# Kernel optimization log

Measured on AMD Instinct MI355X. Metric: run time of the kernel, lower is better.

The kernel has to match this reference:

```python
import jax, jax.numpy as jnp
import numpy as np

D_MODEL = 1024
NUM_HEADS = 16
BATCH = 2
SEQ = 2048


def _trunc_normal(key, shape, std):
    # truncated normal on [-3std, 3std], matching torch.nn.init.trunc_normal_
    return jax.random.truncated_normal(key, -3.0, 3.0, shape, dtype=jnp.float32) * std


def setup_inputs() -> dict:
    key = jax.random.key(0)
    kx, kq, kk, kv, ko = jax.random.split(key, 5)
    std = (2.0 / (D_MODEL + D_MODEL)) ** 0.5
    return {
        "X": jax.random.normal(kx, (BATCH, SEQ, D_MODEL), dtype=jnp.float32),
        "q_proj": _trunc_normal(kq, (D_MODEL, D_MODEL), std),
        "k_proj": _trunc_normal(kk, (D_MODEL, D_MODEL), std),
        "v_proj": _trunc_normal(kv, (D_MODEL, D_MODEL), std),
        "o_proj": _trunc_normal(ko, (D_MODEL, D_MODEL), std),
    }


def reference(X, q_proj, k_proj, v_proj, o_proj):
    B, S, D = X.shape
    H = NUM_HEADS
    d_k = D // H

    # weights stored as (d_model, d_model); split output dim into heads
    q_w = q_proj.reshape(H, d_k, D)        # heads d_k d_model
    k_w = k_proj.reshape(H, d_k, D)
    v_w = v_proj.reshape(H, d_k, D)
    o_w = o_proj.reshape(D, H, d_k).transpose(1, 0, 2)  # heads d_model d_v

    q = jnp.einsum('hkd,bsd->bhsk', q_w, X)  # [B,H,S,d_k]
    k = jnp.einsum('hkd,bsd->bhsk', k_w, X)
    v = jnp.einsum('hkd,bsd->bhsk', v_w, X)

    scale = 1.0 / jnp.sqrt(jnp.asarray(d_k, dtype=X.dtype))
    scores = jnp.einsum('bhqk,bhsk->bhqs', q, k) * scale  # [B,H,S,S]
    causal = jnp.tril(jnp.ones((S, S), dtype=bool))
    scores = jnp.where(causal, scores, jnp.asarray(-jnp.inf, dtype=scores.dtype))
    attn = jax.nn.softmax(scores, axis=-1)
    attn_out = jnp.einsum('bhqs,bhsk->bhqk', attn, v)  # [B,H,S,d_v]

    return jnp.einsum('hdv,bhsv->bsd', o_w, attn_out)  # [B,S,d_model]
```

## Files before the change

### kernel.cpp

```cpp
#include <hip/hip_runtime.h>

typedef unsigned short u16;
typedef __bf16 bf16x8 __attribute__((ext_vector_type(8)));
typedef float f32x4 __attribute__((ext_vector_type(4)));
typedef u16 u16x8 __attribute__((ext_vector_type(8)));
typedef u16 u16x4v __attribute__((ext_vector_type(4)));

#define D_MODEL 1024
#define SEQ 2048
#define NB 2
#define NH 16

#define MFMA(a, b, c) __builtin_amdgcn_mfma_f32_16x16x32_bf16(a, b, c, 0, 0, 0)

__device__ __forceinline__ u16 f2bf(float f) {
  unsigned u = __builtin_bit_cast(unsigned, f);
  u += 0x7FFFu + ((u >> 16) & 1u);
  return (u16)(u >> 16);
}

__device__ __forceinline__ u16 f2bf_hw(float f) {
  return __builtin_bit_cast(u16, (__bf16)f);
}

__device__ __forceinline__ bf16x8 ld8(const u16* p) {
  return __builtin_bit_cast(bf16x8, *(const u16x8*)p);
}

typedef const __attribute__((address_space(1))) unsigned gu32;
typedef __attribute__((address_space(3))) unsigned lu32;
__device__ __forceinline__ void gload16(const u16* g, u16* l) {
  __builtin_amdgcn_global_load_lds((gu32*)g, (lu32*)l, 16, 0, 0);
}

__global__ __launch_bounds__(256) void convert_kernel(
    const float* __restrict__ X, const float* __restrict__ Wq,
    const float* __restrict__ Wk, const float* __restrict__ Wv,
    const float* __restrict__ Wo, u16* __restrict__ Xb, u16* __restrict__ Wb)
{
  const int NX4 = 1024 * 1024;
  const int NW4 = 256 * 1024;
  const int TOT = NX4 + 4 * NW4;
  for (int i = blockIdx.x * 256 + threadIdx.x; i < TOT; i += gridDim.x * 256) {
    const float* src;
    u16* dst;
    if (i < NX4) {
      src = X + (size_t)i * 4;
      dst = Xb + (size_t)i * 4;
    } else {
      int j = i - NX4;
      int w = j >> 18;
      int off = j & (NW4 - 1);
      const float* ws = (w == 0) ? Wq : (w == 1) ? Wk : (w == 2) ? Wv : Wo;
      src = ws + (size_t)off * 4;
      dst = Wb + (size_t)j * 4;
    }
    float4 v = *(const float4*)src;
    u16x4v o = { f2bf(v.x), f2bf(v.y), f2bf(v.z), f2bf(v.w) };
    *(u16x4v*)dst = o;
  }
}

template<int MODE>
__global__ __launch_bounds__(256) void gemm128(
    const u16* __restrict__ A, const u16* __restrict__ B,
    u16* __restrict__ Qb, u16* __restrict__ Kb, u16* __restrict__ Vt,
    float* __restrict__ out)
{
  __shared__ u16 As[2][128 * 64];
  __shared__ u16 Bs[2][128 * 64];
  const int t = threadIdx.x;
  const int lane = t & 63, w = t >> 6;
  const int wr = w >> 1, wc = w & 1;
  const int m0 = blockIdx.x * 128;
  const int n0 = blockIdx.y * 128;
  const int kg = lane >> 4, lr = lane & 15;
  const int lrow = lane >> 3, lch = lane & 7;

  f32x4 acc[4][4] = {};

  auto stage = [&](int buf, int kt) {
    #pragma unroll
    for (int i = 0; i < 4; ++i) {
      int row = (w * 4 + i) * 8 + lrow;
      int sch = lch ^ (row & 7);
      gload16(&A[(size_t)(m0 + row) * 1024 + kt * 64 + sch * 8], &As[buf][(w * 4 + i) * 512]);
      gload16(&B[(size_t)(n0 + row) * 1024 + kt * 64 + sch * 8], &Bs[buf][(w * 4 + i) * 512]);
    }
  };

  stage(0, 0);
  __syncthreads();
  int cur = 0;

  for (int kt = 0; kt < 16; ++kt) {
    if (kt + 1 < 16) stage(cur ^ 1, kt + 1);

    const u16* as = &As[cur][0];
    const u16* bs = &Bs[cur][0];
    #pragma unroll
    for (int kh = 0; kh < 2; ++kh) {
      bf16x8 a[4], b[4];
      #pragma unroll
      for (int mi = 0; mi < 4; ++mi) {
        int row = wr * 64 + mi * 16 + lr;
        int ch = (kh * 4 + kg) ^ (lr & 7);
        a[mi] = ld8(&as[row * 64 + ch * 8]);
      }
      #pragma unroll
      for (int ni = 0; ni < 4; ++ni) {
        int row = wc * 64 + ni * 16 + lr;
        int ch = (kh * 4 + kg) ^ (lr & 7);
        b[ni] = ld8(&bs[row * 64 + ch * 8]);
      }
      #pragma unroll
      for (int mi = 0; mi < 4; ++mi)
        #pragma unroll
        for (int ni = 0; ni < 4; ++ni)
          acc[mi][ni] = MFMA(a[mi], b[ni], acc[mi][ni]);
    }

    __syncthreads();
    cur ^= 1;
  }

  if (MODE == 0) {
    const int zby = blockIdx.y >> 3;
    const int nl0 = (blockIdx.y & 7) * 128;
    const float scl = (zby == 0) ? 0.125f : 1.0f;
    #pragma unroll
    for (int mi = 0; mi < 4; ++mi) {
      #pragma unroll
      for (int ni = 0; ni < 4; ++ni) {
        int m = m0 + wr * 64 + mi * 16 + kg * 4;
        int nl = nl0 + wc * 64 + ni * 16 + lr;
        int bb = m >> 11, s = m & (SEQ - 1);
        int h = nl >> 6, dk = nl & 63;
        size_t bh = (size_t)(bb * NH + h);
        if (zby == 2) {
          u16x4v v = { f2bf(acc[mi][ni][0]), f2bf(acc[mi][ni][1]),
                       f2bf(acc[mi][ni][2]), f2bf(acc[mi][ni][3]) };
          *(u16x4v*)&Vt[(bh * 64 + dk) * SEQ + s] = v;
        } else {
          u16* dst = (zby == 0 ? Qb : Kb) + ((bh * SEQ + s) * 64 + dk);
          #pragma unroll
          for (int i = 0; i < 4; ++i) dst[(size_t)i * 64] = f2bf(acc[mi][ni][i] * scl);
        }
      }
    }
  } else {
    #pragma unroll
    for (int mi = 0; mi < 4; ++mi) {
      #pragma unroll
      for (int ni = 0; ni < 4; ++ni) {
        int m = m0 + wr * 64 + mi * 16 + kg * 4;
        int n = n0 + wc * 64 + ni * 16 + lr;
        #pragma unroll
        for (int i = 0; i < 4; ++i)
          out[(size_t)(m + i) * D_MODEL + n] = acc[mi][ni][i];
      }
    }
  }
}

__global__ __launch_bounds__(256) void attn_kernel(
    const u16* __restrict__ Qb, const u16* __restrict__ Kb,
    const u16* __restrict__ Vt, u16* __restrict__ AO)
{
  __shared__ u16 Ks[2][64 * 64];
  __shared__ u16 Vs[2][64 * 64];
  __shared__ u16 Ps[4][16][72];
  const int t = threadIdx.x;
  const int bh = blockIdx.x;
  const int p = blockIdx.y;
  const int lane = t & 63, wv = t >> 6;
  const int kg = lane >> 4, lr = lane & 15;
  const int r8 = lane >> 3, c = lane & 7;
  const int b = bh >> 4, h = bh & (NH - 1);

  auto stage = [&](int buf, int kv0) {
    #pragma unroll
    for (int i = 0; i < 2; ++i) {
      int s = wv * 2 + i;
      int row = s * 8 + r8;
      int sc = c ^ (row & 7);
      gload16(&Kb[((size_t)bh * SEQ + kv0 + row) * 64 + sc * 8], &Ks[buf][s * 512]);
      gload16(&Vt[((size_t)bh * 64 + row) * SEQ + kv0 + sc * 8], &Vs[buf][s * 512]);
    }
  };

  #pragma unroll 1
  for (int seg = 0; seg < 2; ++seg) {
    const int qt = seg ? (31 - p) : p;
    const int ntile = qt + 1;
    const int q0 = qt * 64;

    const size_t qrow = (size_t)bh * SEQ + q0 + wv * 16 + lr;
    bf16x8 aq0 = ld8(&Qb[qrow * 64 + kg * 8]);
    bf16x8 aq1 = ld8(&Qb[qrow * 64 + 32 + kg * 8]);

    f32x4 of[4] = {};
    float rs[4] = {0.f, 0.f, 0.f, 0.f};

    __syncthreads();
    stage(0, 0);
    int cur = 0;

    for (int kt = 0; kt < ntile; ++kt) {
      const int kv0 = kt * 64;
      __syncthreads();
      if (kt + 1 < ntile) stage(cur ^ 1, (kt + 1) * 64);

      const u16* kb = &Ks[cur][0];
      f32x4 sc4[4] = {};
      #pragma unroll
      for (int ct = 0; ct < 4; ++ct) {
        int ch0 = kg ^ (lr & 7);
        int ch1 = (4 + kg) ^ (lr & 7);
        sc4[ct] = MFMA(aq0, ld8(&kb[(ct * 16 + lr) * 64 + ch0 * 8]), sc4[ct]);
        sc4[ct] = MFMA(aq1, ld8(&kb[(ct * 16 + lr) * 64 + ch1 * 8]), sc4[ct]);
      }

      const bool domask = (kt == ntile - 1);
      #pragma unroll
      for (int ct = 0; ct < 4; ++ct)
        #pragma unroll
        for (int i = 0; i < 4; ++i) {
          float e = __expf(sc4[ct][i]);
          if (domask && (kv0 + ct * 16 + lr > q0 + wv * 16 + kg * 4 + i)) e = 0.f;
          sc4[ct][i] = e;
          rs[i] += e;
        }

      #pragma unroll
      for (int ct = 0; ct < 4; ++ct)
        #pragma unroll
        for (int i = 0; i < 4; ++i)
          Ps[wv][kg * 4 + i][ct * 16 + lr] = f2bf_hw(sc4[ct][i]);

      bf16x8 pa0 = ld8(&Ps[wv][lr][kg * 8]);
      bf16x8 pa1 = ld8(&Ps[wv][lr][32 + kg * 8]);

      const u16* vb = &Vs[cur][0];
      #pragma unroll
      for (int vt = 0; vt < 4; ++vt) {
        int ch0 = kg ^ (lr & 7);
        int ch1 = (4 + kg) ^ (lr & 7);
        of[vt] = MFMA(pa0, ld8(&vb[(vt * 16 + lr) * 64 + ch0 * 8]), of[vt]);
        of[vt] = MFMA(pa1, ld8(&vb[(vt * 16 + lr) * 64 + ch1 * 8]), of[vt]);
      }
      cur ^= 1;
    }

    #pragma unroll
    for (int off = 1; off < 16; off <<= 1)
      #pragma unroll
      for (int i = 0; i < 4; ++i)
        rs[i] += __shfl_xor(rs[i], off, 64);

    #pragma unroll
    for (int i = 0; i < 4; ++i) {
      float inv = 1.0f / rs[i];
      int s = q0 + wv * 16 + kg * 4 + i;
      size_t base = ((size_t)(b * SEQ + s)) * D_MODEL + h * 64 + lr;
      #pragma unroll
      for (int vt = 0; vt < 4; ++vt)
        AO[base + vt * 16] = f2bf_hw(of[vt][i] * inv);
    }
  }
}

extern "C" void kernel_launch(void* const* d_in, const int* in_sizes, int n_in,
                              void* d_out, int out_size, void* d_ws, size_t ws_size,
                              hipStream_t stream) {
  const float* X  = (const float*)d_in[0];
  const float* Wq = (const float*)d_in[1];
  const float* Wk = (const float*)d_in[2];
  const float* Wv = (const float*)d_in[3];
  const float* Wo = (const float*)d_in[4];
  float* out = (float*)d_out;

  u16* Xb = (u16*)d_ws;
  u16* Wb = Xb + (size_t)4096 * 1024;
  u16* Qb = Wb + (size_t)4096 * 1024;
  u16* Kb = Qb + (size_t)4096 * 1024;
  u16* Vt = Kb + (size_t)4096 * 1024;
  u16* AO = Vt + (size_t)4096 * 1024;

  convert_kernel<<<2048, 256, 0, stream>>>(X, Wq, Wk, Wv, Wo, Xb, Wb);
  gemm128<0><<<dim3(32, 24), 256, 0, stream>>>(Xb, Wb, Qb, Kb, Vt, nullptr);
  attn_kernel<<<dim3(32, 16), 256, 0, stream>>>(Qb, Kb, Vt, AO);
  gemm128<1><<<dim3(32, 8), 256, 0, stream>>>(AO, Wb + (size_t)3 * 1024 * 1024,
                                              nullptr, nullptr, nullptr, out);
}
```

Before: 115.1 us.

## Replace QKV GEMM with 256x256 eight-wave kernel using a four-stage async pipeline

The QKV projection moves to a new 512-thread kernel with 256x256 tiles, BK=32, and four LDS buffers filled by global_load_lds. Loads are issued three tiles ahead, with explicit vmcnt waits and barriers in place of the old double-buffered loop. The aim is to hide global memory latency and raise MFMA reuse per loaded tile. MFMA sections in this GEMM and in attention are also wrapped in s_setprio to favour matrix-issuing waves. The grid shrinks to 192 blocks and LDS use grows, so fewer blocks can cover the GPU's compute units.

```diff
diff --git a/kernel.cpp b/kernel.cpp
--- a/kernel.cpp
+++ b/kernel.cpp
@@ -32,6 +32,12 @@
 __device__ __forceinline__ void gload16(const u16* g, u16* l) {
   __builtin_amdgcn_global_load_lds((gu32*)g, (lu32*)l, 16, 0, 0);
 }
+
+#define WAITV8 asm volatile("s_waitcnt vmcnt(8)" ::: "memory")
+#define WAITV4 asm volatile("s_waitcnt vmcnt(4)" ::: "memory")
+#define WAITV0 asm volatile("s_waitcnt vmcnt(0)" ::: "memory")
+#define BARRIER __builtin_amdgcn_s_barrier()
+#define SB0 __builtin_amdgcn_sched_barrier(0)
 
 __global__ __launch_bounds__(256) void convert_kernel(
     const float* __restrict__ X, const float* __restrict__ Wq,
@@ -61,10 +67,103 @@
   }
 }
 
-template<int MODE>
-__global__ __launch_bounds__(256) void gemm128(
+__global__ __launch_bounds__(512, 2) void qkv8w(
     const u16* __restrict__ A, const u16* __restrict__ B,
-    u16* __restrict__ Qb, u16* __restrict__ Kb, u16* __restrict__ Vt,
+    u16* __restrict__ Qb, u16* __restrict__ Kb, u16* __restrict__ Vt)
+{
+  __shared__ u16 As[4][8192];
+  __shared__ u16 Bs[4][8192];
+  const int t = threadIdx.x;
+  const int lane = t & 63, w = t >> 6;
+  const int wm = w >> 2, wn = w & 3;
+  const int m0 = blockIdx.x * 256;
+  const int n0 = blockIdx.y * 256;
+  const int kg = lane >> 4, lr = lane & 15;
+  const int rp = lr >> 1, hf = lr & 1;
+  const int xr = (((hf * 4 + kg) ^ rp) * 8);
+
+  const int lc = (lane & 7) ^ (lane >> 3);
+  const int ghalf = lc >> 2, kc = lc & 3;
+
+  f32x4 acc[8][4] = {};
+
+  auto stage = [&](int buf, int kt) {
+    #pragma unroll
+    for (int j = 0; j < 2; ++j) {
+      int g = (j * 64 + w * 8 + (lane >> 3)) * 2 + ghalf;
+      gload16(&A[(size_t)(m0 + g) * 1024 + kt * 32 + kc * 8],
+              &As[buf][(j * 8 + w) * 512]);
+      gload16(&B[(size_t)(n0 + g) * 1024 + kt * 32 + kc * 8],
+              &Bs[buf][(j * 8 + w) * 512]);
+    }
+  };
+
+  auto phase = [&](int buf) {
+    const u16* as = &As[buf][0];
+    const u16* bs = &Bs[buf][0];
+    bf16x8 a[8], b[4];
+    #pragma unroll
+    for (int mi = 0; mi < 8; ++mi)
+      a[mi] = ld8(&as[(wm * 64 + mi * 8 + rp) * 64 + xr]);
+    #pragma unroll
+    for (int ni = 0; ni < 4; ++ni)
+      b[ni] = ld8(&bs[(wn * 32 + ni * 8 + rp) * 64 + xr]);
+    __builtin_amdgcn_s_setprio(1);
+    #pragma unroll
+    for (int mi = 0; mi < 8; ++mi)
+      #pragma unroll
+      for (int ni = 0; ni < 4; ++ni)
+        acc[mi][ni] = MFMA(a[mi], b[ni], acc[mi][ni]);
+    __builtin_amdgcn_s_setprio(0);
+  };
+
+  stage(0, 0);
+  stage(1, 1);
+  stage(2, 2);
+
+  for (int tt = 0; tt < 28; tt += 4) {
+    #pragma unroll
+    for (int q = 0; q < 4; ++q) {
+      const int kt = tt + q;
+      WAITV8;
+      BARRIER;
+      SB0;
+      stage((q + 3) & 3, kt + 3);
+      phase(q);
+    }
+  }
+  WAITV8; BARRIER; SB0; stage(3, 31); phase(0);
+  WAITV8; BARRIER; SB0; phase(1);
+  WAITV4; BARRIER; SB0; phase(2);
+  WAITV0; BARRIER; SB0; phase(3);
+
+  const int zby = blockIdx.y >> 2;
+  const int nl0 = (blockIdx.y & 3) * 256;
+  const float scl = (zby == 0) ? 0.125f : 1.0f;
+  #pragma unroll
+  for (int mi = 0; mi < 8; ++mi) {
+    #pragma unroll
+    for (int ni = 0; ni < 4; ++ni) {
+      int m = m0 + wm * 128 + mi * 16 + kg * 4;
+      int nl = nl0 + wn * 64 + ni * 16 + lr;
+      int bb = m >> 11, s = m & (SEQ - 1);
+      int h = nl >> 6, dk = nl & 63;
+      size_t bh = (size_t)(bb * NH + h);
+      if (zby == 2) {
+        u16x4v v = { f2bf(acc[mi][ni][0]), f2bf(acc[mi][ni][1]),
+                     f2bf(acc[mi][ni][2]), f2bf(acc[mi][ni][3]) };
+        *(u16x4v*)&Vt[(bh * 64 + dk) * SEQ + s] = v;
+      } else {
+        u16* dst = (zby == 0 ? Qb : Kb) + ((bh * SEQ + s) * 64 + dk);
+        #pragma unroll
+        for (int i = 0; i < 4; ++i) dst[(size_t)i * 64] = f2bf(acc[mi][ni][i] * scl);
+      }
+    }
+  }
+}
+
+__global__ __launch_bounds__(256) void oproj_kernel(
+    const u16* __restrict__ A, const u16* __restrict__ B,
     float* __restrict__ out)
 {
   __shared__ u16 As[2][128 * 64];
@@ -124,41 +223,15 @@
     cur ^= 1;
   }
 
-  if (MODE == 0) {
-    const int zby = blockIdx.y >> 3;
-    const int nl0 = (blockIdx.y & 7) * 128;
-    const float scl = (zby == 0) ? 0.125f : 1.0f;
-    #pragma unroll
-    for (int mi = 0; mi < 4; ++mi) {
-      #pragma unroll
-      for (int ni = 0; ni < 4; ++ni) {
-        int m = m0 + wr * 64 + mi * 16 + kg * 4;
-        int nl = nl0 + wc * 64 + ni * 16 + lr;
-        int bb = m >> 11, s = m & (SEQ - 1);
-        int h = nl >> 6, dk = nl & 63;
-        size_t bh = (size_t)(bb * NH + h);
-        if (zby == 2) {
-          u16x4v v = { f2bf(acc[mi][ni][0]), f2bf(acc[mi][ni][1]),
-                       f2bf(acc[mi][ni][2]), f2bf(acc[mi][ni][3]) };
-          *(u16x4v*)&Vt[(bh * 64 + dk) * SEQ + s] = v;
-        } else {
-          u16* dst = (zby == 0 ? Qb : Kb) + ((bh * SEQ + s) * 64 + dk);
-          #pragma unroll
-          for (int i = 0; i < 4; ++i) dst[(size_t)i * 64] = f2bf(acc[mi][ni][i] * scl);
-        }
-      }
-    }
-  } else {
-    #pragma unroll
-    for (int mi = 0; mi < 4; ++mi) {
-      #pragma unroll
-      for (int ni = 0; ni < 4; ++ni) {
-        int m = m0 + wr * 64 + mi * 16 + kg * 4;
-        int n = n0 + wc * 64 + ni * 16 + lr;
-        #pragma unroll
-        for (int i = 0; i < 4; ++i)
-          out[(size_t)(m + i) * D_MODEL + n] = acc[mi][ni][i];
-      }
+  #pragma unroll
+  for (int mi = 0; mi < 4; ++mi) {
+    #pragma unroll
+    for (int ni = 0; ni < 4; ++ni) {
+      int m = m0 + wr * 64 + mi * 16 + kg * 4;
+      int n = n0 + wc * 64 + ni * 16 + lr;
+      #pragma unroll
+      for (int i = 0; i < 4; ++i)
+        out[(size_t)(m + i) * D_MODEL + n] = acc[mi][ni][i];
     }
   }
 }
@@ -213,6 +286,7 @@
 
       const u16* kb = &Ks[cur][0];
       f32x4 sc4[4] = {};
+      __builtin_amdgcn_s_setprio(1);
       #pragma unroll
       for (int ct = 0; ct < 4; ++ct) {
         int ch0 = kg ^ (lr & 7);
@@ -220,6 +294,7 @@
         sc4[ct] = MFMA(aq0, ld8(&kb[(ct * 16 + lr) * 64 + ch0 * 8]), sc4[ct]);
         sc4[ct] = MFMA(aq1, ld8(&kb[(ct * 16 + lr) * 64 + ch1 * 8]), sc4[ct]);
       }
+      __builtin_amdgcn_s_setprio(0);
 
       const bool domask = (kt == ntile - 1);
       #pragma unroll
@@ -242,6 +317,7 @@
       bf16x8 pa1 = ld8(&Ps[wv][lr][32 + kg * 8]);
 
       const u16* vb = &Vs[cur][0];
+      __builtin_amdgcn_s_setprio(1);
       #pragma unroll
       for (int vt = 0; vt < 4; ++vt) {
         int ch0 = kg ^ (lr & 7);
@@ -249,6 +325,7 @@
         of[vt] = MFMA(pa0, ld8(&vb[(vt * 16 + lr) * 64 + ch0 * 8]), of[vt]);
         of[vt] = MFMA(pa1, ld8(&vb[(vt * 16 + lr) * 64 + ch1 * 8]), of[vt]);
       }
+      __builtin_amdgcn_s_setprio(0);
       cur ^= 1;
     }
 
@@ -288,8 +365,7 @@
   u16* AO = Vt + (size_t)4096 * 1024;
 
   convert_kernel<<<2048, 256, 0, stream>>>(X, Wq, Wk, Wv, Wo, Xb, Wb);
-  gemm128<0><<<dim3(32, 24), 256, 0, stream>>>(Xb, Wb, Qb, Kb, Vt, nullptr);
+  qkv8w<<<dim3(16, 12), 512, 0, stream>>>(Xb, Wb, Qb, Kb, Vt);
   attn_kernel<<<dim3(32, 16), 256, 0, stream>>>(Qb, Kb, Vt, AO);
-  gemm128<1><<<dim3(32, 8), 256, 0, stream>>>(AO, Wb + (size_t)3 * 1024 * 1024,
-                                              nullptr, nullptr, nullptr, out);
-}
+  oproj_kernel<<<dim3(32, 8), 256, 0, stream>>>(AO, Wb + (size_t)3 * 1024 * 1024, out);
+}
```

Result: faster. 110.2 us (-4.3%).
